# Kernel tuning notes

Measured on AMD Instinct MI355X. Metric: run time of the kernel, lower is better.

The kernel has to match this reference:

```python
import jax, jax.numpy as jnp
import numpy as np

N_NODES = 100000
N_EDGES = 1600000
HIDDEN = 128
N_LAYERS = 4
EPS = 0.0  # GINConv default eps, train_eps=False


def setup_inputs() -> dict:
    key = jax.random.key(0)
    ks = jax.random.split(key, 6)
    scale = 1.0 / np.sqrt(HIDDEN)
    return {
        "x": jax.random.normal(ks[0], (N_NODES, HIDDEN), dtype=jnp.float32),
        "edge_index": jax.random.randint(ks[1], (2, N_EDGES), 0, N_NODES, dtype=jnp.int64),
        "W1": jax.random.normal(ks[2], (N_LAYERS, HIDDEN, HIDDEN), dtype=jnp.float32) * scale,
        "b1": jnp.zeros((N_LAYERS, HIDDEN), dtype=jnp.float32),
        "W2": jax.random.normal(ks[3], (N_LAYERS, HIDDEN, HIDDEN), dtype=jnp.float32) * scale,
        "b2": jnp.zeros((N_LAYERS, HIDDEN), dtype=jnp.float32),
    }


def reference(x, edge_index, W1, b1, W2, b2):
    src = edge_index[0]  # message sources (x_j)
    dst = edge_index[1]  # aggregation targets
    n = x.shape[0]
    for l in range(N_LAYERS):
        x_in = x
        # scatter-add aggregation: sum_{j in N(i)} x_j
        agg = jax.ops.segment_sum(x[src], dst, num_segments=n)
        out = agg + (1.0 + EPS) * x
        # GIN MLP: Linear -> ReLU -> Linear
        h = jax.nn.relu(out @ W1[l] + b1[l]) @ W2[l] + b2[l]
        # outer loop: relu, dropout (identity in eval), residual
        x = x_in + jax.nn.relu(h)
    return x
```

## Files before the change

kernel.cpp:

```cpp
#include <hip/hip_runtime.h>

typedef unsigned short u16;
typedef unsigned int u32;
typedef unsigned char u8;

constexpr int NN = 100000;
constexpr int NE = 1600000;
constexpr int H = 128;

constexpr int NB = 196;
constexpr int BCAP = 10240;
constexpr int PB_E = 4096;
constexpr int PB_BLOCKS = (NE + PB_E - 1) / PB_E;

typedef __bf16 bf16x8 __attribute__((ext_vector_type(8)));
typedef float f32x16 __attribute__((ext_vector_type(16)));

__device__ __forceinline__ u16 f2bf(float f) {
    union { float f; u32 u; } cv; cv.f = f;
    u32 r = (cv.u + 0x7fffu + ((cv.u >> 16) & 1u)) >> 16;
    return (u16)r;
}
__device__ __forceinline__ float bflo(u32 u) {
    union { u32 u; float f; } cv; cv.u = u << 16; return cv.f;
}
__device__ __forceinline__ float bfhi(u32 u) {
    union { u32 u; float f; } cv; cv.u = u & 0xffff0000u; return cv.f;
}

__global__ __launch_bounds__(256) void part_kernel(const int* __restrict__ e,
                                                   int* __restrict__ gcursor,
                                                   u32* __restrict__ ebuf) {
    __shared__ int lcnt[256];
    __shared__ int ps[256];
    __shared__ int ex[256];
    __shared__ int gbaseL[NB];
    __shared__ int anynz;
    __shared__ u32 sbuf[PB_E];
    __shared__ u8 sbk[PB_E];
    const int t = threadIdx.x;
    if (t == 0) anynz = 0;
    lcnt[t] = 0;
    __syncthreads();
    int loc = 0;
    for (int i = t; i < 4096; i += 256) loc |= e[2 * i + 1];
    if (loc) atomicOr(&anynz, 1);
    __syncthreads();
    const int st = anynz ? 1 : 2;
    const int base = blockIdx.x * PB_E;
    const int nval = (NE - base < PB_E) ? (NE - base) : PB_E;
    u32 pk[16]; int bk[16]; int rk[16];
#pragma unroll
    for (int j = 0; j < 16; ++j) {
        int i = base + j * 256 + t;
        bk[j] = -1;
        if (i < NE) {
            int s = e[st * i];
            int d = e[st * (NE + i)];
            int b = d >> 9;
            pk[j] = (u32)s | ((u32)(d & 511) << 17);
            bk[j] = b;
            rk[j] = atomicAdd(&lcnt[b], 1);
        }
    }
    __syncthreads();
    int v = lcnt[t];
    ps[t] = v;
    __syncthreads();
    for (int off = 1; off < 256; off <<= 1) {
        int u = (t >= off) ? ps[t - off] : 0;
        __syncthreads();
        ps[t] += u;
        __syncthreads();
    }
    ex[t] = ps[t] - v;
    if (t < NB && v > 0) gbaseL[t] = atomicAdd(&gcursor[t], v);
    __syncthreads();
#pragma unroll
    for (int j = 0; j < 16; ++j)
        if (bk[j] >= 0) {
            int p = ex[bk[j]] + rk[j];
            sbuf[p] = pk[j];
            sbk[p] = (u8)bk[j];
        }
    __syncthreads();
    for (int i = t; i < nval; i += 256) {
        int b = sbk[i];
        ebuf[b * BCAP + gbaseL[b] + (i - ex[b])] = sbuf[i];
    }
}

__global__ __launch_bounds__(256) void bscan_kernel(const int* __restrict__ gcursor,
                                                    int* __restrict__ bbase,
                                                    int* __restrict__ offs) {
    __shared__ int s[256];
    int t = threadIdx.x;
    int v = (t < NB) ? gcursor[t] : 0;
    s[t] = v;
    __syncthreads();
    for (int off = 1; off < 256; off <<= 1) {
        int u = (t >= off) ? s[t - off] : 0;
        __syncthreads();
        s[t] += u;
        __syncthreads();
    }
    if (t < NB) bbase[t] = s[t] - v;
    if (t == 0) offs[NN] = NE;
}

__global__ __launch_bounds__(256) void bfill_kernel(const u32* __restrict__ ebuf,
                                                    const int* __restrict__ gcursor,
                                                    const int* __restrict__ bbase,
                                                    int* __restrict__ offs,
                                                    int* __restrict__ colv) {
    __shared__ int ncnt[512];
    __shared__ int cur[512];
    __shared__ int ps[256];
    const int b = blockIdx.x, t = threadIdx.x;
    const int En = gcursor[b];
    const int bb = bbase[b];
    ncnt[t] = 0; ncnt[t + 256] = 0;
    __syncthreads();
    const u32* eb = ebuf + b * BCAP;
    for (int i = t; i < En; i += 256)
        atomicAdd(&ncnt[eb[i] >> 17], 1);
    __syncthreads();
    int s2 = ncnt[2 * t] + ncnt[2 * t + 1];
    ps[t] = s2;
    __syncthreads();
    for (int off = 1; off < 256; off <<= 1) {
        int u = (t >= off) ? ps[t - off] : 0;
        __syncthreads();
        ps[t] += u;
        __syncthreads();
    }
    int e0 = ps[t] - s2;
    cur[2 * t] = e0;
    cur[2 * t + 1] = e0 + ncnt[2 * t];
    __syncthreads();
    const int n0 = b * 512;
    for (int i = t; i < 512; i += 256)
        if (n0 + i < NN) offs[n0 + i] = bb + cur[i];
    __syncthreads();
    for (int i = t; i < En; i += 256) {
        u32 p = eb[i];
        int pos = atomicAdd(&cur[p >> 17], 1);
        colv[bb + pos] = (int)((p & 0x1FFFFu) | (((p >> 17) & 31u) << 27));
    }
}

__global__ void init_kernel(const float* __restrict__ W1,
                            const float* __restrict__ W2,
                            u16* __restrict__ wt,
                            const float* __restrict__ xin,
                            float* __restrict__ x, u16* __restrict__ xb) {
    int b = blockIdx.x;
    if (b < 512) {
        int t = b * 256 + threadIdx.x;
        int w = t >> 14;
        int r = t & 16383;
        int k = r >> 7, n = r & 127;
        int l = w >> 1, s = w & 1;
        const float* src = (s == 0 ? W1 : W2) + l * 16384;
        wt[w * 16384 + n * 128 + k] = f2bf(src[k * 128 + n]);
    } else {
        int i = (b - 512) * 256 + threadIdx.x;
        float4 v = ((const float4*)xin)[i];
        ((float4*)x)[i] = v;
        uint2 p;
        p.x = (u32)f2bf(v.x) | ((u32)f2bf(v.y) << 16);
        p.y = (u32)f2bf(v.z) | ((u32)f2bf(v.w) << 16);
        ((uint2*)xb)[i] = p;
    }
}

__global__ __launch_bounds__(256) void mlp_kernel(const u16* __restrict__ xbin,
                                                  const int* __restrict__ colv,
                                                  const int* __restrict__ offs,
                                                  const u16* __restrict__ wt1,
                                                  const u16* __restrict__ wt2,
                                                  const float* __restrict__ b1,
                                                  const float* __restrict__ b2,
                                                  float* __restrict__ x,
                                                  u16* __restrict__ xbout) {
    __shared__ u16 lds[32 * 128];
    const int tid = threadIdx.x;
    const int wave = tid >> 6, lane = tid & 63;
    const int ml = lane & 31, g = lane >> 5;
    const int row0 = blockIdx.x * 32;

    bf16x8 bfrag[8];
#pragma unroll
    for (int ks = 0; ks < 8; ++ks)
        bfrag[ks] = *(const bf16x8*)(wt1 + (wave * 32 + ml) * H + ks * 16 + g * 8);
    const float bias1 = b1[wave * 32 + ml];
    const float bias2 = b2[wave * 32 + ml];

#pragma unroll
    for (int i = 0; i < 2; ++i) {
        int ch = tid + 256 * i;
        int r = ch >> 4, c = ch & 15;
        int gr = row0 + r;
        int4 v = *(const int4*)(xbin + gr * H + c * 8);
        *(int4*)(&lds[r * H + ((c ^ (r & 15)) << 3)]) = v;
    }
    __syncthreads();

    {
        const int node0 = row0 + wave * 8;
        const int jb = __builtin_amdgcn_readfirstlane(offs[node0]);
        const int je = __builtin_amdgcn_readfirstlane(offs[node0 + 8]);
        int cur = wave * 8;
        float a0 = 0.f, a1 = 0.f;
        if (jb < je) {
            u32 ce[16];
#pragma unroll
            for (int q = 0; q < 16; ++q) {
                int idx = jb + q;
                idx = idx < je ? idx : je - 1;
                ce[q] = (u32)__builtin_amdgcn_readfirstlane(colv[idx]);
            }
            for (int j = jb; j < je; j += 16) {
                u32 uu[16];
#pragma unroll
                for (int q = 0; q < 16; ++q)
                    uu[q] = *(const u32*)(xbin + (ce[q] & 0x1FFFFu) * H + lane * 2);
                u32 cn[16];
#pragma unroll
                for (int q = 0; q < 16; ++q) {
                    int idx = j + 16 + q;
                    idx = idx < je ? idx : je - 1;
                    cn[q] = (u32)__builtin_amdgcn_readfirstlane(colv[idx]);
                }
#pragma unroll
                for (int q = 0; q < 16; ++q) {
                    if (j + q < je) {
                        int rloc = (int)(ce[q] >> 27);
                        if (rloc != cur) {
                            u16* p = &lds[cur * H + (((lane >> 2) ^ (cur & 15)) << 3) + ((lane & 3) << 1)];
                            u32 old = *(u32*)p;
                            *(u32*)p = (u32)f2bf(bflo(old) + a0) | ((u32)f2bf(bfhi(old) + a1) << 16);
                            a0 = 0.f; a1 = 0.f; cur = rloc;
                        }
                        a0 += bflo(uu[q]); a1 += bfhi(uu[q]);
                    }
                }
#pragma unroll
                for (int q = 0; q < 16; ++q) ce[q] = cn[q];
            }
        }
        u16* p = &lds[cur * H + (((lane >> 2) ^ (cur & 15)) << 3) + ((lane & 3) << 1)];
        u32 old = *(u32*)p;
        *(u32*)p = (u32)f2bf(bflo(old) + a0) | ((u32)f2bf(bfhi(old) + a1) << 16);
    }

    __syncthreads();

    f32x16 acc;
#pragma unroll
    for (int i = 0; i < 16; ++i) acc[i] = 0.f;

#pragma unroll
    for (int ks = 0; ks < 8; ++ks) {
        int chunk = (2 * ks + g) ^ (ml & 15);
        bf16x8 afrag = *(const bf16x8*)(&lds[ml * H + (chunk << 3)]);
        acc = __builtin_amdgcn_mfma_f32_32x32x16_bf16(afrag, bfrag[ks], acc, 0, 0, 0);
    }

    __syncthreads();

#pragma unroll
    for (int reg = 0; reg < 16; ++reg) {
        int rm = (reg & 3) + ((reg >> 2) << 3) + 4 * g;
        int cn = wave * 32 + ml;
        float v = acc[reg] + bias1;
        v = v > 0.f ? v : 0.f;
        lds[rm * H + ((((cn >> 3) ^ (rm & 15))) << 3) + (cn & 7)] = f2bf(v);
    }

#pragma unroll
    for (int ks = 0; ks < 8; ++ks)
        bfrag[ks] = *(const bf16x8*)(wt2 + (wave * 32 + ml) * H + ks * 16 + g * 8);

#pragma unroll
    for (int i = 0; i < 16; ++i) acc[i] = 0.f;

    __syncthreads();

#pragma unroll
    for (int ks = 0; ks < 8; ++ks) {
        int chunk = (2 * ks + g) ^ (ml & 15);
        bf16x8 afrag = *(const bf16x8*)(&lds[ml * H + (chunk << 3)]);
        acc = __builtin_amdgcn_mfma_f32_32x32x16_bf16(afrag, bfrag[ks], acc, 0, 0, 0);
    }

    __syncthreads();

#pragma unroll
    for (int reg = 0; reg < 16; ++reg) {
        int rm = (reg & 3) + ((reg >> 2) << 3) + 4 * g;
        int cn = wave * 32 + ml;
        float v = acc[reg] + bias2;
        v = v > 0.f ? v : 0.f;
        lds[rm * H + ((((cn >> 3) ^ (rm & 15))) << 3) + (cn & 7)] = f2bf(v);
    }

    __syncthreads();

#pragma unroll
    for (int i = 0; i < 2; ++i) {
        int ch = tid + 256 * i;
        int r = ch >> 4, c = ch & 15;
        int gr = row0 + r;
        int4 hv = *(const int4*)(&lds[r * H + ((c ^ (r & 15)) << 3)]);
        float4 x0 = *(const float4*)(x + gr * H + c * 8);
        float4 x1 = *(const float4*)(x + gr * H + c * 8 + 4);
        x0.x += bflo((u32)hv.x); x0.y += bfhi((u32)hv.x);
        x0.z += bflo((u32)hv.y); x0.w += bfhi((u32)hv.y);
        x1.x += bflo((u32)hv.z); x1.y += bfhi((u32)hv.z);
        x1.z += bflo((u32)hv.w); x1.w += bfhi((u32)hv.w);
        *(float4*)(x + gr * H + c * 8) = x0;
        *(float4*)(x + gr * H + c * 8 + 4) = x1;
        int4 xo;
        xo.x = (int)((u32)f2bf(x0.x) | ((u32)f2bf(x0.y) << 16));
        xo.y = (int)((u32)f2bf(x0.z) | ((u32)f2bf(x0.w) << 16));
        xo.z = (int)((u32)f2bf(x1.x) | ((u32)f2bf(x1.y) << 16));
        xo.w = (int)((u32)f2bf(x1.z) | ((u32)f2bf(x1.w) << 16));
        *(int4*)(xbout + gr * H + c * 8) = xo;
    }
}

extern "C" void kernel_launch(void* const* d_in, const int* in_sizes, int n_in,
                              void* d_out, int out_size, void* d_ws, size_t ws_size,
                              hipStream_t stream) {
    const float* x_in = (const float*)d_in[0];
    const int* edges = (const int*)d_in[1];
    const float* W1 = (const float*)d_in[2];
    const float* b1 = (const float*)d_in[3];
    const float* W2 = (const float*)d_in[4];
    const float* b2 = (const float*)d_in[5];
    float* x = (float*)d_out;

    char* ws = (char*)d_ws;
    int* gcursor = (int*)(ws + 512);
    int* bbase = (int*)(ws + 2048);
    int* offs = (int*)(ws + 4096);
    int* colv = (int*)(ws + 406528);
    u16* wt = (u16*)(ws + 6809600);
    u16* xb0 = (u16*)(ws + 7072768);
    u16* xb1 = (u16*)(ws + 32672768);
    u32* ebuf = (u32*)xb1;

    hipMemsetAsync(gcursor, 0, NB * sizeof(int), stream);
    part_kernel<<<PB_BLOCKS, 256, 0, stream>>>(edges, gcursor, ebuf);
    bscan_kernel<<<1, 256, 0, stream>>>(gcursor, bbase, offs);
    bfill_kernel<<<NB, 256, 0, stream>>>(ebuf, gcursor, bbase, offs, colv);
    init_kernel<<<512 + (NN * H / 4) / 256, 256, 0, stream>>>(W1, W2, wt, x_in, x, xb0);

    for (int l = 0; l < 4; ++l) {
        u16* xin = (l & 1) ? xb1 : xb0;
        u16* xout = (l & 1) ? xb0 : xb1;
        mlp_kernel<<<NN / 32, 256, 0, stream>>>(
            xin, colv, offs,
            wt + (l * 2) * 16384, wt + (l * 2 + 1) * 16384,
            b1 + l * 128, b2 + l * 128, x, xout);
    }
}
```

Measured before the change: 485.5 us.

## Store residual as bf16 hi/lo pair and fuse preprocessing kernels

```diff
diff --git a/kernel.cpp b/kernel.cpp
--- a/kernel.cpp
+++ b/kernel.cpp
@@ -12,6 +12,8 @@
 constexpr int BCAP = 10240;
 constexpr int PB_E = 4096;
 constexpr int PB_BLOCKS = (NE + PB_E - 1) / PB_E;
+constexpr int WT_BLOCKS = 512;
+constexpr int XI_BLOCKS = (NN * H / 4) / 256;
 
 typedef __bf16 bf16x8 __attribute__((ext_vector_type(8)));
 typedef float f32x16 __attribute__((ext_vector_type(16)));
@@ -27,10 +29,21 @@
 __device__ __forceinline__ float bfhi(u32 u) {
     union { u32 u; float f; } cv; cv.u = u & 0xffff0000u; return cv.f;
 }
-
-__global__ __launch_bounds__(256) void part_kernel(const int* __restrict__ e,
-                                                   int* __restrict__ gcursor,
-                                                   u32* __restrict__ ebuf) {
+__device__ __forceinline__ u32 pkbf(float a, float b) {
+    return (u32)f2bf(a) | ((u32)f2bf(b) << 16);
+}
+
+__global__ __launch_bounds__(256) void preproc_kernel(const int* __restrict__ e,
+                                                      int* __restrict__ gcursor,
+                                                      u32* __restrict__ ebuf,
+                                                      const float* __restrict__ W1,
+                                                      const float* __restrict__ W2,
+                                                      u16* __restrict__ wt,
+                                                      const float* __restrict__ xin,
+                                                      float* __restrict__ x,
+                                                      u16* __restrict__ xb,
+                                                      u16* __restrict__ xe,
+                                                      int mode) {
     __shared__ int lcnt[256];
     __shared__ int ps[256];
     __shared__ int ex[256];
@@ -38,7 +51,37 @@
     __shared__ int anynz;
     __shared__ u32 sbuf[PB_E];
     __shared__ u8 sbk[PB_E];
+    const int blk = blockIdx.x;
     const int t = threadIdx.x;
+
+    if (blk >= PB_BLOCKS) {
+        if (blk < PB_BLOCKS + WT_BLOCKS) {
+            int tt = (blk - PB_BLOCKS) * 256 + t;
+            int w = tt >> 14;
+            int r = tt & 16383;
+            int k = r >> 7, n = r & 127;
+            int l = w >> 1, s = w & 1;
+            const float* src = (s == 0 ? W1 : W2) + l * 16384;
+            wt[w * 16384 + n * 128 + k] = f2bf(src[k * 128 + n]);
+        } else {
+            int i = (blk - PB_BLOCKS - WT_BLOCKS) * 256 + t;
+            float4 v = ((const float4*)xin)[i];
+            uint2 p;
+            p.x = pkbf(v.x, v.y);
+            p.y = pkbf(v.z, v.w);
+            ((uint2*)xb)[i] = p;
+            if (mode == 1) {
+                uint2 q;
+                q.x = pkbf(v.x - bflo(p.x), v.y - bfhi(p.x));
+                q.y = pkbf(v.z - bflo(p.y), v.w - bfhi(p.y));
+                ((uint2*)xe)[i] = q;
+            } else {
+                ((float4*)x)[i] = v;
+            }
+        }
+        return;
+    }
+
     if (t == 0) anynz = 0;
     lcnt[t] = 0;
     __syncthreads();
@@ -47,7 +90,7 @@
     if (loc) atomicOr(&anynz, 1);
     __syncthreads();
     const int st = anynz ? 1 : 2;
-    const int base = blockIdx.x * PB_E;
+    const int base = blk * PB_E;
     const int nval = (NE - base < PB_E) ? (NE - base) : PB_E;
     u32 pk[16]; int bk[16]; int rk[16];
 #pragma unroll
@@ -90,27 +133,8 @@
     }
 }
 
-__global__ __launch_bounds__(256) void bscan_kernel(const int* __restrict__ gcursor,
-                                                    int* __restrict__ bbase,
-                                                    int* __restrict__ offs) {
-    __shared__ int s[256];
-    int t = threadIdx.x;
-    int v = (t < NB) ? gcursor[t] : 0;
-    s[t] = v;
-    __syncthreads();
-    for (int off = 1; off < 256; off <<= 1) {
-        int u = (t >= off) ? s[t - off] : 0;
-        __syncthreads();
-        s[t] += u;
-        __syncthreads();
-    }
-    if (t < NB) bbase[t] = s[t] - v;
-    if (t == 0) offs[NN] = NE;
-}
-
 __global__ __launch_bounds__(256) void bfill_kernel(const u32* __restrict__ ebuf,
                                                     const int* __restrict__ gcursor,
-                                                    const int* __restrict__ bbase,
                                                     int* __restrict__ offs,
                                                     int* __restrict__ colv) {
     __shared__ int ncnt[512];
@@ -118,7 +142,17 @@
     __shared__ int ps[256];
     const int b = blockIdx.x, t = threadIdx.x;
     const int En = gcursor[b];
-    const int bb = bbase[b];
+    int gv = (t < NB) ? gcursor[t] : 0;
+    ps[t] = gv;
+    __syncthreads();
+    for (int off = 1; off < 256; off <<= 1) {
+        int u = (t >= off) ? ps[t - off] : 0;
+        __syncthreads();
+        ps[t] += u;
+        __syncthreads();
+    }
+    const int bb = ps[b] - En;
+    if (b == 0 && t == 0) offs[NN] = NE;
     ncnt[t] = 0; ncnt[t + 256] = 0;
     __syncthreads();
     const u32* eb = ebuf + b * BCAP;
@@ -149,31 +183,7 @@
     }
 }
 
-__global__ void init_kernel(const float* __restrict__ W1,
-                            const float* __restrict__ W2,
-                            u16* __restrict__ wt,
-                            const float* __restrict__ xin,
-                            float* __restrict__ x, u16* __restrict__ xb) {
-    int b = blockIdx.x;
-    if (b < 512) {
-        int t = b * 256 + threadIdx.x;
-        int w = t >> 14;
-        int r = t & 16383;
-        int k = r >> 7, n = r & 127;
-        int l = w >> 1, s = w & 1;
-        const float* src = (s == 0 ? W1 : W2) + l * 16384;
-        wt[w * 16384 + n * 128 + k] = f2bf(src[k * 128 + n]);
-    } else {
-        int i = (b - 512) * 256 + threadIdx.x;
-        float4 v = ((const float4*)xin)[i];
-        ((float4*)x)[i] = v;
-        uint2 p;
-        p.x = (u32)f2bf(v.x) | ((u32)f2bf(v.y) << 16);
-        p.y = (u32)f2bf(v.z) | ((u32)f2bf(v.w) << 16);
-        ((uint2*)xb)[i] = p;
-    }
-}
-
+template <int MODE, bool LAST>
 __global__ __launch_bounds__(256) void mlp_kernel(const u16* __restrict__ xbin,
                                                   const int* __restrict__ colv,
                                                   const int* __restrict__ offs,
@@ -182,26 +192,22 @@
                                                   const float* __restrict__ b1,
                                                   const float* __restrict__ b2,
                                                   float* __restrict__ x,
-                                                  u16* __restrict__ xbout) {
+                                                  u16* __restrict__ xbout,
+                                                  u16* __restrict__ xe) {
     __shared__ u16 lds[32 * 128];
     const int tid = threadIdx.x;
     const int wave = tid >> 6, lane = tid & 63;
     const int ml = lane & 31, g = lane >> 5;
     const int row0 = blockIdx.x * 32;
 
-    bf16x8 bfrag[8];
-#pragma unroll
-    for (int ks = 0; ks < 8; ++ks)
-        bfrag[ks] = *(const bf16x8*)(wt1 + (wave * 32 + ml) * H + ks * 16 + g * 8);
-    const float bias1 = b1[wave * 32 + ml];
-    const float bias2 = b2[wave * 32 + ml];
-
+    int4 sv[2];
 #pragma unroll
     for (int i = 0; i < 2; ++i) {
         int ch = tid + 256 * i;
         int r = ch >> 4, c = ch & 15;
         int gr = row0 + r;
         int4 v = *(const int4*)(xbin + gr * H + c * 8);
+        sv[i] = v;
         *(int4*)(&lds[r * H + ((c ^ (r & 15)) << 3)]) = v;
     }
     __syncthreads();
@@ -239,7 +245,7 @@
                         if (rloc != cur) {
                             u16* p = &lds[cur * H + (((lane >> 2) ^ (cur & 15)) << 3) + ((lane & 3) << 1)];
                             u32 old = *(u32*)p;
-                            *(u32*)p = (u32)f2bf(bflo(old) + a0) | ((u32)f2bf(bfhi(old) + a1) << 16);
+                            *(u32*)p = pkbf(bflo(old) + a0, bfhi(old) + a1);
                             a0 = 0.f; a1 = 0.f; cur = rloc;
                         }
                         a0 += bflo(uu[q]); a1 += bfhi(uu[q]);
@@ -251,8 +257,15 @@
         }
         u16* p = &lds[cur * H + (((lane >> 2) ^ (cur & 15)) << 3) + ((lane & 3) << 1)];
         u32 old = *(u32*)p;
-        *(u32*)p = (u32)f2bf(bflo(old) + a0) | ((u32)f2bf(bfhi(old) + a1) << 16);
-    }
+        *(u32*)p = pkbf(bflo(old) + a0, bfhi(old) + a1);
+    }
+
+    bf16x8 bfrag[8];
+#pragma unroll
+    for (int ks = 0; ks < 8; ++ks)
+        bfrag[ks] = *(const bf16x8*)(wt1 + (wave * 32 + ml) * H + ks * 16 + g * 8);
+    const float bias1 = b1[wave * 32 + ml];
+    const float bias2 = b2[wave * 32 + ml];
 
     __syncthreads();
 
@@ -313,20 +326,53 @@
         int r = ch >> 4, c = ch & 15;
         int gr = row0 + r;
         int4 hv = *(const int4*)(&lds[r * H + ((c ^ (r & 15)) << 3)]);
-        float4 x0 = *(const float4*)(x + gr * H + c * 8);
-        float4 x1 = *(const float4*)(x + gr * H + c * 8 + 4);
-        x0.x += bflo((u32)hv.x); x0.y += bfhi((u32)hv.x);
-        x0.z += bflo((u32)hv.y); x0.w += bfhi((u32)hv.y);
-        x1.x += bflo((u32)hv.z); x1.y += bfhi((u32)hv.z);
-        x1.z += bflo((u32)hv.w); x1.w += bfhi((u32)hv.w);
-        *(float4*)(x + gr * H + c * 8) = x0;
-        *(float4*)(x + gr * H + c * 8 + 4) = x1;
-        int4 xo;
-        xo.x = (int)((u32)f2bf(x0.x) | ((u32)f2bf(x0.y) << 16));
-        xo.y = (int)((u32)f2bf(x0.z) | ((u32)f2bf(x0.w) << 16));
-        xo.z = (int)((u32)f2bf(x1.x) | ((u32)f2bf(x1.y) << 16));
-        xo.w = (int)((u32)f2bf(x1.z) | ((u32)f2bf(x1.w) << 16));
-        *(int4*)(xbout + gr * H + c * 8) = xo;
+        if constexpr (MODE == 1) {
+            int4 se = sv[i];
+            int4 le = *(const int4*)(xe + gr * H + c * 8);
+            float xn[8];
+            xn[0] = bflo((u32)se.x) + bflo((u32)le.x) + bflo((u32)hv.x);
+            xn[1] = bfhi((u32)se.x) + bfhi((u32)le.x) + bfhi((u32)hv.x);
+            xn[2] = bflo((u32)se.y) + bflo((u32)le.y) + bflo((u32)hv.y);
+            xn[3] = bfhi((u32)se.y) + bfhi((u32)le.y) + bfhi((u32)hv.y);
+            xn[4] = bflo((u32)se.z) + bflo((u32)le.z) + bflo((u32)hv.z);
+            xn[5] = bfhi((u32)se.z) + bfhi((u32)le.z) + bfhi((u32)hv.z);
+            xn[6] = bflo((u32)se.w) + bflo((u32)le.w) + bflo((u32)hv.w);
+            xn[7] = bfhi((u32)se.w) + bfhi((u32)le.w) + bfhi((u32)hv.w);
+            if constexpr (LAST) {
+                float4 o0 = make_float4(xn[0], xn[1], xn[2], xn[3]);
+                float4 o1 = make_float4(xn[4], xn[5], xn[6], xn[7]);
+                *(float4*)(x + gr * H + c * 8) = o0;
+                *(float4*)(x + gr * H + c * 8 + 4) = o1;
+            } else {
+                int4 ho, lo4;
+                u32 h0, h1;
+                h0 = pkbf(xn[0], xn[1]); ho.x = (int)h0;
+                lo4.x = (int)pkbf(xn[0] - bflo(h0), xn[1] - bfhi(h0));
+                h1 = pkbf(xn[2], xn[3]); ho.y = (int)h1;
+                lo4.y = (int)pkbf(xn[2] - bflo(h1), xn[3] - bfhi(h1));
+                h0 = pkbf(xn[4], xn[5]); ho.z = (int)h0;
+                lo4.z = (int)pkbf(xn[4] - bflo(h0), xn[5] - bfhi(h0));
+                h1 = pkbf(xn[6], xn[7]); ho.w = (int)h1;
+                lo4.w = (int)pkbf(xn[6] - bflo(h1), xn[7] - bfhi(h1));
+                *(int4*)(xbout + gr * H + c * 8) = ho;
+                *(int4*)(xe + gr * H + c * 8) = lo4;
+            }
+        } else {
+            float4 x0 = *(const float4*)(x + gr * H + c * 8);
+            float4 x1 = *(const float4*)(x + gr * H + c * 8 + 4);
+            x0.x += bflo((u32)hv.x); x0.y += bfhi((u32)hv.x);
+            x0.z += bflo((u32)hv.y); x0.w += bfhi((u32)hv.y);
+            x1.x += bflo((u32)hv.z); x1.y += bfhi((u32)hv.z);
+            x1.z += bflo((u32)hv.w); x1.w += bfhi((u32)hv.w);
+            *(float4*)(x + gr * H + c * 8) = x0;
+            *(float4*)(x + gr * H + c * 8 + 4) = x1;
+            int4 xo;
+            xo.x = (int)pkbf(x0.x, x0.y);
+            xo.y = (int)pkbf(x0.z, x0.w);
+            xo.z = (int)pkbf(x1.x, x1.y);
+            xo.w = (int)pkbf(x1.z, x1.w);
+            *(int4*)(xbout + gr * H + c * 8) = xo;
+        }
     }
 }
 
@@ -343,26 +389,39 @@
 
     char* ws = (char*)d_ws;
     int* gcursor = (int*)(ws + 512);
-    int* bbase = (int*)(ws + 2048);
     int* offs = (int*)(ws + 4096);
     int* colv = (int*)(ws + 406528);
     u16* wt = (u16*)(ws + 6809600);
     u16* xb0 = (u16*)(ws + 7072768);
     u16* xb1 = (u16*)(ws + 32672768);
+    u16* xe = (u16*)(ws + 58272768);
     u32* ebuf = (u32*)xb1;
 
+    const bool big = ws_size >= (size_t)83872768;
+    const int mode = big ? 1 : 0;
+
     hipMemsetAsync(gcursor, 0, NB * sizeof(int), stream);
-    part_kernel<<<PB_BLOCKS, 256, 0, stream>>>(edges, gcursor, ebuf);
-    bscan_kernel<<<1, 256, 0, stream>>>(gcursor, bbase, offs);
-    bfill_kernel<<<NB, 256, 0, stream>>>(ebuf, gcursor, bbase, offs, colv);
-    init_kernel<<<512 + (NN * H / 4) / 256, 256, 0, stream>>>(W1, W2, wt, x_in, x, xb0);
+    preproc_kernel<<<PB_BLOCKS + WT_BLOCKS + XI_BLOCKS, 256, 0, stream>>>(
+        edges, gcursor, ebuf, W1, W2, wt, x_in, x, xb0, xe, mode);
+    bfill_kernel<<<NB, 256, 0, stream>>>(ebuf, gcursor, offs, colv);
 
     for (int l = 0; l < 4; ++l) {
         u16* xin = (l & 1) ? xb1 : xb0;
         u16* xout = (l & 1) ? xb0 : xb1;
-        mlp_kernel<<<NN / 32, 256, 0, stream>>>(
-            xin, colv, offs,
-            wt + (l * 2) * 16384, wt + (l * 2 + 1) * 16384,
-            b1 + l * 128, b2 + l * 128, x, xout);
-    }
-}
+        const u16* w1p = wt + (l * 2) * 16384;
+        const u16* w2p = wt + (l * 2 + 1) * 16384;
+        const float* b1p = b1 + l * 128;
+        const float* b2p = b2 + l * 128;
+        if (big) {
+            if (l < 3)
+                mlp_kernel<1, false><<<NN / 32, 256, 0, stream>>>(
+                    xin, colv, offs, w1p, w2p, b1p, b2p, x, xout, xe);
+            else
+                mlp_kernel<1, true><<<NN / 32, 256, 0, stream>>>(
+                    xin, colv, offs, w1p, w2p, b1p, b2p, x, xout, xe);
+        } else {
+            mlp_kernel<0, false><<<NN / 32, 256, 0, stream>>>(
+                xin, colv, offs, w1p, w2p, b1p, b2p, x, xout, xb0 );
+        }
+    }
+}
```

After: 464.9 us. 1.04x faster.
